# Optimization experiments

Hardware: AMD Instinct MI355X
Metric: run time of the kernel (lower is better)

## Reference

```python
import jax, jax.numpy as jnp
import numpy as np


def setup_inputs() -> dict:
    key = jax.random.key(0)
    ks = jax.random.split(key, 7)
    b, t, c = 2, 2048, 1024
    s = 0.02  # keep pre-softmax logits in a sane range
    return {
        "query": jax.random.normal(ks[0], (b, t, c), jnp.float32),
        "key": jax.random.normal(ks[1], (b, t, c), jnp.float32),
        "value": jax.random.normal(ks[2], (b, t, c), jnp.float32),
        "in_proj_w": jax.random.normal(ks[3], (3 * c, c), jnp.float32) * s,
        "in_proj_b": jax.random.normal(ks[4], (3 * c,), jnp.float32) * s,
        "out_proj_w": jax.random.normal(ks[5], (c, c), jnp.float32) * s,
        "out_proj_b": jax.random.normal(ks[6], (c,), jnp.float32) * s,
        "window_size": 128,
    }


def reference(query, key, value, in_proj_w, in_proj_b, out_proj_w, out_proj_b, window_size):
    num_heads = 16
    b, t, c = query.shape
    hd = c // num_heads
    wq, wk, wv = in_proj_w[:c], in_proj_w[c:2 * c], in_proj_w[2 * c:]
    bq, bk, bv = in_proj_b[:c], in_proj_b[c:2 * c], in_proj_b[2 * c:]
    # project and split heads: [b, h, t, hd]
    q = (query @ wq.T + bq).reshape(b, t, num_heads, hd).transpose(0, 2, 1, 3)
    k = (key @ wk.T + bk).reshape(b, t, num_heads, hd).transpose(0, 2, 1, 3)
    v = (value @ wv.T + bv).reshape(b, t, num_heads, hd).transpose(0, 2, 1, 3)
    # NOTE: torch adds a *float* attn_mask to the logits. The original mask is
    # 1.0 inside the sliding window, 0.0 outside -- an additive +1 bias, NOT -inf.
    idx = jnp.arange(t)
    band = (jnp.abs(idx[:, None] - idx[None, :]) <= window_size).astype(q.dtype)  # [t, t]
    scale = 1.0 / jnp.sqrt(jnp.asarray(hd, q.dtype))
    logits = jnp.einsum("bhqd,bhkd->bhqk", q * scale, k) + band  # [b,h,t,t]
    attn = jax.nn.softmax(logits, axis=-1)
    out = jnp.einsum("bhqk,bhkd->bhqd", attn, v)  # [b,h,t,hd]
    out = out.transpose(0, 2, 1, 3).reshape(b, t, c)
    return out @ out_proj_w.T + out_proj_b
```

## Files before the change

### kernel.cpp

```cpp
#include <hip/hip_runtime.h>

typedef __attribute__((ext_vector_type(8)))  short short8;
typedef __attribute__((ext_vector_type(4)))  float f32x4;
typedef __attribute__((ext_vector_type(16))) float f32x16;
typedef __attribute__((ext_vector_type(2)))  unsigned uint2v;

constexpr int B  = 2;
constexpr int T  = 2048;
constexpr int C  = 1024;
constexpr int H  = 16;
constexpr int HD = 64;

__device__ inline unsigned bf16rne(float a){
  unsigned u = __builtin_bit_cast(unsigned, a);
  u += 0x7fffu + ((u >> 16) & 1u);
  return u >> 16;
}
__device__ inline unsigned bf16pair(float a, float b){
  unsigned ua = __builtin_bit_cast(unsigned, a); ua += 0x7fffu + ((ua >> 16) & 1u);
  unsigned ub = __builtin_bit_cast(unsigned, b); ub += 0x7fffu + ((ub >> 16) & 1u);
  return (ua >> 16) | (ub & 0xffff0000u);
}
__device__ inline void gll16(const void* g, void* l){
  __builtin_amdgcn_global_load_lds(
      (const __attribute__((address_space(1))) unsigned*)g,
      (__attribute__((address_space(3))) unsigned*)l, 16, 0, 0);
}
__device__ inline float exp2f_(float x){
#if __has_builtin(__builtin_amdgcn_exp2f)
  return __builtin_amdgcn_exp2f(x);
#else
  return __builtin_exp2f(x);
#endif
}

__global__ void convert_k(const float* __restrict__ ipw, const float* __restrict__ opw,
                          const float* __restrict__ q, const float* __restrict__ k,
                          const float* __restrict__ v, unsigned* __restrict__ dst)
{
  const int i = blockIdx.x * 256 + threadIdx.x;
  const long e = (long)i * 4;
  const float* src; long off;
  if      (e <  3145728) { src = ipw; off = e; }
  else if (e <  4194304) { src = opw; off = e - 3145728; }
  else if (e <  8388608) { src = q;   off = e - 4194304; }
  else if (e < 12582912) { src = k;   off = e - 8388608; }
  else                   { src = v;   off = e - 12582912; }
  const float4 x = *(const float4*)(src + off);
  dst[i*2+0] = bf16pair(x.x, x.y);
  dst[i*2+1] = bf16pair(x.z, x.w);
}

__global__ __launch_bounds__(256, 3) void gemm_qkv(
    const unsigned short* __restrict__ A0, const unsigned short* __restrict__ A1,
    const unsigned short* __restrict__ A2,
    const unsigned short* __restrict__ Wb, const float* __restrict__ bias,
    unsigned short* __restrict__ Qb, unsigned short* __restrict__ Kf,
    unsigned short* __restrict__ Vf)
{
  __shared__ __align__(16) char gsm[32768];
  unsigned short* As = (unsigned short*)gsm;
  unsigned short* Bs = (unsigned short*)(gsm + 16384);

  const int tid  = threadIdx.x, lane = tid & 63, wv = tid >> 6;
  const int wm   = wv & 1, wn = wv >> 1;
  const int bn   = blockIdx.x, bm = blockIdx.y;
  const int m16  = lane & 15, quad = lane >> 4;

  const int which = bn >> 3;
  const unsigned short* A = (which == 0) ? A0 : (which == 1 ? A1 : A2);

  f32x4 acc[4][4];
#pragma unroll
  for (int i = 0; i < 4; i++)
#pragma unroll
    for (int j = 0; j < 4; j++) acc[i][j] = (f32x4){0.f, 0.f, 0.f, 0.f};

  const int srow = wv * 32 + (lane >> 3);
  const int skp  = (lane & 7) * 8;

  for (int k0 = 0; k0 < 1024; k0 += 64) {
    __syncthreads();
#pragma unroll
    for (int p = 0; p < 4; p++) {
      gll16(A  + (size_t)(bm*128 + srow + p*8)*1024 + k0 + skp, (char*)As + wv*4096 + p*1024);
      gll16(Wb + (size_t)(bn*128 + srow + p*8)*1024 + k0 + skp, (char*)Bs + wv*4096 + p*1024);
    }
    __syncthreads();

#pragma unroll
    for (int kk = 0; kk < 2; kk++) {
      short8 af[4], bf[4];
#pragma unroll
      for (int i = 0; i < 4; i++)
        af[i] = *(const short8*)((const char*)As + (wm*64 + i*16 + m16)*128 + kk*64 + quad*16);
#pragma unroll
      for (int j = 0; j < 4; j++)
        bf[j] = *(const short8*)((const char*)Bs + (wn*64 + j*16 + m16)*128 + kk*64 + quad*16);
#pragma unroll
      for (int i = 0; i < 4; i++)
#pragma unroll
        for (int j = 0; j < 4; j++)
          acc[i][j] = __builtin_amdgcn_mfma_f32_16x16x32_bf16(af[i], bf[j], acc[i][j], 0,0,0);
    }
  }

  __syncthreads();
  float* Ls = (float*)gsm;
  const int hbase = (bn & 7) * 2;
  const int b = bm >> 4;
  const int tbase = (bm & 15) * 128;
  const float ksc = (which == 1) ? 0.18033688f : 1.0f;

  if (which < 2) {
#pragma unroll
    for (int j = 0; j < 4; ++j) {
      const float bj = bias[bn*128 + wn*64 + j*16 + m16] * ksc;
#pragma unroll
      for (int i = 0; i < 4; ++i) {
        const int m0 = wm*64 + i*16 + quad*4;
#pragma unroll
        for (int r = 0; r < 4; ++r)
          Ls[(m0 + r)*36 + wn*16 + m16] = __builtin_fmaf(acc[i][j][r], ksc, bj);
      }
      __syncthreads();
#pragma unroll
      for (int r2 = 0; r2 < 2; ++r2) {
        const int v = r2*256 + tid;
        const int m = v & 127, seg = v >> 7;
        const int wn2 = seg >> 1;
        const float* src = &Ls[m*36 + wn2*16 + (seg & 1)*8];
        const float4 f0 = *(const float4*)src;
        const float4 f1 = *(const float4*)(src + 4);
        uint4 st;
        st.x = bf16pair(f0.x, f0.y); st.y = bf16pair(f0.z, f0.w);
        st.z = bf16pair(f1.x, f1.y); st.w = bf16pair(f1.z, f1.w);
        const int bhh = b*16 + hbase + wn2;
        if (which == 0) {
          const int d0 = j*16 + (seg & 1)*8;
          *(uint4*)&Qb[((size_t)(bhh*2048) + tbase + m)*64 + d0] = st;
        } else {
          const int kt = (tbase + m) >> 6;
          const int wkk = (m >> 5) & 1, ln2 = m & 31;
          const int h2 = seg & 1;
          uint4* dp = (uint4*)Kf + ((size_t)(bhh*32 + kt)*8 + j*2 + wkk)*64 + h2*32 + ln2;
          *dp = st;
        }
      }
      __syncthreads();
    }
  } else {
#pragma unroll
    for (int j = 0; j < 4; ++j) {
      const float bj = bias[bn*128 + wn*64 + j*16 + m16];
      const int col = wn*16 + m16;
#pragma unroll
      for (int i = 0; i < 4; ++i) {
        f32x4 tv = acc[i][j];
        tv[0] += bj; tv[1] += bj; tv[2] += bj; tv[3] += bj;
        *(f32x4*)&Ls[col*132 + wm*64 + i*16 + quad*4] = tv;
      }
      __syncthreads();
#pragma unroll
      for (int r2 = 0; r2 < 2; ++r2) {
        const int v = r2*256 + tid;
        const int n = v >> 4, mseg = v & 15;
        const float* src = &Ls[n*132 + mseg*8];
        const float4 f0 = *(const float4*)src;
        const float4 f1 = *(const float4*)(src + 4);
        uint4 st;
        st.x = bf16pair(f0.x, f0.y); st.y = bf16pair(f0.z, f0.w);
        st.z = bf16pair(f1.x, f1.y); st.w = bf16pair(f1.z, f1.w);
        const int d = j*16 + (n & 15);
        const int bhh = b*16 + hbase + (n >> 4);
        const int t0 = tbase + mseg*8;
        const int kt = t0 >> 6, tc = (t0 & 63) >> 3;
        const int wkk = tc >> 2, cc = (tc >> 1) & 1, h2 = tc & 1;
        const int dt = d >> 5, ln2 = d & 31;
        uint4* dp = (uint4*)Vf + (size_t)(bhh*32 + kt)*512 + dt*256 + cc*128 + wkk*64 + h2*32 + ln2;
        *dp = st;
      }
      __syncthreads();
    }
  }
}

__global__ __launch_bounds__(256, 3) void gemm_out(
    const unsigned short* __restrict__ Ab, const unsigned short* __restrict__ Wb,
    const float* __restrict__ bias, float* __restrict__ outF)
{
  __shared__ __align__(16) char gsm[24576];
  unsigned short* As = (unsigned short*)gsm;
  unsigned short* Ws = (unsigned short*)(gsm + 16384);

  const int tid  = threadIdx.x, lane = tid & 63, wv = tid >> 6;
  const int wm   = wv & 1, wn = wv >> 1;
  const int bn   = blockIdx.x, bm = blockIdx.y;
  const int m16  = lane & 15, quad = lane >> 4;

  f32x4 acc[4][2];
#pragma unroll
  for (int i = 0; i < 4; i++)
#pragma unroll
    for (int j = 0; j < 2; j++) acc[i][j] = (f32x4){0.f, 0.f, 0.f, 0.f};

  const int arow = wv * 32 + (lane >> 3);
  const int wrow = wv * 16 + (lane >> 3);
  const int skp  = (lane & 7) * 8;

  for (int k0 = 0; k0 < 1024; k0 += 64) {
    __syncthreads();
#pragma unroll
    for (int p = 0; p < 4; p++)
      gll16(Ab + (size_t)(bm*128 + arow + p*8)*1024 + k0 + skp, (char*)As + wv*4096 + p*1024);
#pragma unroll
    for (int p = 0; p < 2; p++)
      gll16(Wb + (size_t)(bn*64 + wrow + p*8)*1024 + k0 + skp, (char*)Ws + wv*2048 + p*1024);
    __syncthreads();

#pragma unroll
    for (int kk = 0; kk < 2; kk++) {
      short8 af[4], bf[2];
#pragma unroll
      for (int i = 0; i < 4; i++)
        af[i] = *(const short8*)((const char*)As + (wm*64 + i*16 + m16)*128 + kk*64 + quad*16);
#pragma unroll
      for (int j = 0; j < 2; j++)
        bf[j] = *(const short8*)((const char*)Ws + (wn*32 + j*16 + m16)*128 + kk*64 + quad*16);
#pragma unroll
      for (int i = 0; i < 4; i++)
#pragma unroll
        for (int j = 0; j < 2; j++)
          acc[i][j] = __builtin_amdgcn_mfma_f32_16x16x32_bf16(af[i], bf[j], acc[i][j], 0,0,0);
    }
  }

#pragma unroll
  for (int j = 0; j < 2; j++) {
    const int n_e = bn*64 + wn*32 + j*16 + m16;
    const float bj = bias[n_e];
#pragma unroll
    for (int i = 0; i < 4; i++) {
      const int mbase = bm*128 + wm*64 + i*16 + quad*4;
#pragma unroll
      for (int r = 0; r < 4; r++)
        outF[(size_t)(mbase + r) * 1024 + n_e] = acc[i][j][r] + bj;
    }
  }
}

__global__ __launch_bounds__(256, 3) void attn_k(
    const unsigned short* __restrict__ Qb, const unsigned short* __restrict__ Kf,
    const unsigned short* __restrict__ Vf, const int* __restrict__ wptr,
    unsigned short* __restrict__ ctx)
{
  __shared__ __align__(16) char smem[16896];
  float* Om   = (float*)smem;
  float* lbuf = (float*)(smem + 16384);

  const int tid = threadIdx.x, lane = tid & 63, wv = tid >> 6;
  const int wq = wv >> 1, wk = wv & 1;
  const int h = lane >> 5, ln = lane & 31;
  const int bh = blockIdx.x, qt = blockIdx.y;
  const int win = *wptr;
  const int q0 = qt * 64 + wq * 32;
  const size_t hb = (size_t)bh * T * HD;

  constexpr float LOG2E = 1.44269504f;

  short8 qf[4];
#pragma unroll
  for (int s = 0; s < 4; s++)
    qf[s] = *(const short8*)(Qb + hb + (size_t)(q0 + ln)*64 + s*16 + h*8);

  short8 onesv;
#pragma unroll
  for (int jj = 0; jj < 8; jj++) onesv[jj] = (short)0x3F80;

  f32x16 O0, O1, Lacc, Zv;
#pragma unroll
  for (int r = 0; r < 16; r++) { O0[r] = 0.f; O1[r] = 0.f; Lacc[r] = 0.f; Zv[r] = 0.f; }
  const int tq = q0 + ln;

  const uint4* kbase = (const uint4*)Kf + (size_t)bh*32*512 + wk*64 + lane;
  const uint4* vbase = (const uint4*)Vf + (size_t)bh*32*512 + wk*64 + lane;

  uint4 kA[4], vA[4];
#pragma unroll
  for (int s = 0; s < 4; s++) kA[s] = kbase[s*128];
#pragma unroll
  for (int u = 0; u < 4; u++) vA[u] = vbase[(u >> 1)*256 + (u & 1)*128];

  for (int kt = 0; kt < 32; ++kt) {
    f32x16 st;
#pragma unroll
    for (int s = 0; s < 4; s++) {
      const short8 kf2 = __builtin_bit_cast(short8, kA[s]);
      st = __builtin_amdgcn_mfma_f32_32x32x16_bf16(kf2, qf[s], (s == 0 ? Zv : st), 0, 0, 0);
    }
    if (kt < 31) {
      const size_t o = (size_t)(kt + 1) * 512;
#pragma unroll
      for (int s = 0; s < 4; s++) kA[s] = kbase[o + s*128];
    }

    const int kb = kt*64 + wk*32;
    int sep = 0;
    if (kb > q0 + 31) sep = kb - (q0 + 31);
    else if (q0 > kb + 31) sep = q0 - (kb + 31);
    const int d1 = kb + 31 - q0, d2 = q0 + 31 - kb;
    const int dmax = max(d1 < 0 ? -d1 : d1, d2 < 0 ? -d2 : d2);

    float pr[16];
    if (sep > win) {
#pragma unroll
      for (int r = 0; r < 16; r++) pr[r] = exp2f_(st[r]);
    } else if (dmax <= win) {
#pragma unroll
      for (int r = 0; r < 16; r++) pr[r] = exp2f_(st[r] + LOG2E);
    } else {
      const int tkb = kb + 4*h;
#pragma unroll
      for (int r = 0; r < 16; r++) {
        const int tk = tkb + (r & 3) + 8*(r >> 2);
        int dd = tq - tk; dd = dd < 0 ? -dd : dd;
        pr[r] = exp2f_(st[r] + (dd <= win ? LOG2E : 0.0f));
      }
    }

    unsigned pk[8];
#pragma unroll
    for (int g = 0; g < 8; g++)
      pk[g] = __builtin_amdgcn_perm(__builtin_bit_cast(unsigned, pr[2*g+1]),
                                    __builtin_bit_cast(unsigned, pr[2*g]),
                                    0x07060302u);

#pragma unroll
    for (int c = 0; c < 2; c++) {
      const uint2v s02 = __builtin_amdgcn_permlane32_swap(pk[4*c+0], pk[4*c+2], false, false);
      const uint2v s13 = __builtin_amdgcn_permlane32_swap(pk[4*c+1], pk[4*c+3], false, false);
      union { unsigned u[4]; short8 v; } P;
      P.u[0] = s02[0];
      P.u[1] = s13[0];
      P.u[2] = s02[1];
      P.u[3] = s13[1];
#pragma unroll
      for (int dt = 0; dt < 2; dt++) {
        const short8 vf2 = __builtin_bit_cast(short8, vA[dt*2 + c]);
        if (dt == 0) O0 = __builtin_amdgcn_mfma_f32_32x32x16_bf16(P.v, vf2, O0, 0,0,0);
        else         O1 = __builtin_amdgcn_mfma_f32_32x32x16_bf16(P.v, vf2, O1, 0,0,0);
      }
      Lacc = __builtin_amdgcn_mfma_f32_32x32x16_bf16(P.v, onesv, Lacc, 0,0,0);
    }

    if (kt < 31) {
      const size_t o = (size_t)(kt + 1) * 512;
#pragma unroll
      for (int u = 0; u < 4; u++) vA[u] = vbase[o + (u >> 1)*256 + (u & 1)*128];
    }
  }

  __syncthreads();
  if (wk == 1) {
#pragma unroll
    for (int r = 0; r < 16; r++) {
      Om[wq*2048 + r*64 + lane]        = O0[r];
      Om[wq*2048 + (16 + r)*64 + lane] = O1[r];
    }
    if (ln == 0) {
#pragma unroll
      for (int r = 0; r < 16; r++)
        lbuf[wq*32 + (r & 3) + 8*(r >> 2) + 4*h] = Lacc[r];
    }
  }
  __syncthreads();
  if (wk == 0) {
    const int b = bh >> 4, hh = bh & 15;
#pragma unroll
    for (int r = 0; r < 16; r++) {
      const int qrow = (r & 3) + 8*(r >> 2) + 4*h;
      const float lt = Lacc[r] + lbuf[wq*32 + qrow];
      const float linv = 1.0f / lt;
      const int t = q0 + qrow;
      const float o0 = (O0[r] + Om[wq*2048 + r*64 + lane]) * linv;
      const float o1 = (O1[r] + Om[wq*2048 + (16 + r)*64 + lane]) * linv;
      unsigned short* cp = ctx + (size_t)(b*2048 + t)*1024 + hh*64;
      cp[ln]      = (unsigned short)bf16rne(o0);
      cp[32 + ln] = (unsigned short)bf16rne(o1);
    }
  }
}

extern "C" void kernel_launch(void* const* d_in, const int* in_sizes, int n_in,
                              void* d_out, int out_size, void* d_ws, size_t ws_size,
                              hipStream_t stream)
{
  const float* query = (const float*)d_in[0];
  const float* key   = (const float*)d_in[1];
  const float* value = (const float*)d_in[2];
  const float* ipw   = (const float*)d_in[3];
  const float* ipb   = (const float*)d_in[4];
  const float* opw   = (const float*)d_in[5];
  const float* opb   = (const float*)d_in[6];
  const int*   win   = (const int*)d_in[7];

  char* ws = (char*)d_ws;
  unsigned short* Winbf  = (unsigned short*)(ws);
  unsigned short* Woutbf = (unsigned short*)(ws + 6291456);
  unsigned short* Qin    = (unsigned short*)(ws + 8388608);
  unsigned short* Kin    = (unsigned short*)(ws + 16777216);
  unsigned short* Vin    = (unsigned short*)(ws + 25165824);
  unsigned short* Qb     = (unsigned short*)(ws + 33554432);
  unsigned short* Kf     = (unsigned short*)(ws + 41943040);
  unsigned short* Vf     = (unsigned short*)(ws + 50331648);
  unsigned short* ctx    = (unsigned short*)(ws + 58720256);

  convert_k<<<16384, 256, 0, stream>>>(ipw, opw, query, key, value, (unsigned*)ws);

  gemm_qkv<<<dim3(24, 32), 256, 0, stream>>>(
      Qin, Kin, Vin, Winbf, ipb, Qb, Kf, Vf);

  attn_k<<<dim3(32, 32), 256, 0, stream>>>(Qb, Kf, Vf, win, ctx);

  gemm_out<<<dim3(16, 32), 256, 0, stream>>>(
      ctx, Woutbf, opb, (float*)d_out);
}
```

Before: 221.0 us.

## Widen convert stores, shrink out-proj GEMM tiles, split attention launch by batch

The conversion kernel now processes 8 floats per thread and writes one 16-byte store, halving the grid. The output projection GEMM moves from 128x64 to 64x64 tiles with each wave owning a 16-column strip, which doubles the block count and cuts LDS so 4 blocks fit per CU. The attention launch is split into two launches of 16 batch-heads each via an offset argument. Smaller GEMM tiles improve occupancy and wave balance but lower per-block data reuse, and the extra attention launch adds launch overhead.

```diff
diff --git a/kernel.cpp b/kernel.cpp
--- a/kernel.cpp
+++ b/kernel.cpp
@@ -39,16 +39,19 @@
                           const float* __restrict__ v, unsigned* __restrict__ dst)
 {
   const int i = blockIdx.x * 256 + threadIdx.x;
-  const long e = (long)i * 4;
+  const long e = (long)i * 8;
   const float* src; long off;
   if      (e <  3145728) { src = ipw; off = e; }
   else if (e <  4194304) { src = opw; off = e - 3145728; }
   else if (e <  8388608) { src = q;   off = e - 4194304; }
   else if (e < 12582912) { src = k;   off = e - 8388608; }
   else                   { src = v;   off = e - 12582912; }
-  const float4 x = *(const float4*)(src + off);
-  dst[i*2+0] = bf16pair(x.x, x.y);
-  dst[i*2+1] = bf16pair(x.z, x.w);
+  const float4 x0 = *(const float4*)(src + off);
+  const float4 x1 = *(const float4*)(src + off + 4);
+  uint4 st;
+  st.x = bf16pair(x0.x, x0.y); st.y = bf16pair(x0.z, x0.w);
+  st.z = bf16pair(x1.x, x1.y); st.w = bf16pair(x1.z, x1.w);
+  *(uint4*)(dst + (size_t)i*4) = st;
 }
 
 __global__ __launch_bounds__(256, 3) void gemm_qkv(
@@ -185,74 +188,62 @@
   }
 }
 
-__global__ __launch_bounds__(256, 3) void gemm_out(
+__global__ __launch_bounds__(256, 4) void gemm_out(
     const unsigned short* __restrict__ Ab, const unsigned short* __restrict__ Wb,
     const float* __restrict__ bias, float* __restrict__ outF)
 {
-  __shared__ __align__(16) char gsm[24576];
+  __shared__ __align__(16) char gsm[16384];
   unsigned short* As = (unsigned short*)gsm;
-  unsigned short* Ws = (unsigned short*)(gsm + 16384);
+  unsigned short* Ws = (unsigned short*)(gsm + 8192);
 
   const int tid  = threadIdx.x, lane = tid & 63, wv = tid >> 6;
-  const int wm   = wv & 1, wn = wv >> 1;
   const int bn   = blockIdx.x, bm = blockIdx.y;
   const int m16  = lane & 15, quad = lane >> 4;
 
-  f32x4 acc[4][2];
-#pragma unroll
-  for (int i = 0; i < 4; i++)
-#pragma unroll
-    for (int j = 0; j < 2; j++) acc[i][j] = (f32x4){0.f, 0.f, 0.f, 0.f};
-
-  const int arow = wv * 32 + (lane >> 3);
-  const int wrow = wv * 16 + (lane >> 3);
+  f32x4 acc[4];
+#pragma unroll
+  for (int i = 0; i < 4; i++) acc[i] = (f32x4){0.f, 0.f, 0.f, 0.f};
+
+  const int srow = wv * 16 + (lane >> 3);
   const int skp  = (lane & 7) * 8;
 
   for (int k0 = 0; k0 < 1024; k0 += 64) {
     __syncthreads();
 #pragma unroll
-    for (int p = 0; p < 4; p++)
-      gll16(Ab + (size_t)(bm*128 + arow + p*8)*1024 + k0 + skp, (char*)As + wv*4096 + p*1024);
-#pragma unroll
-    for (int p = 0; p < 2; p++)
-      gll16(Wb + (size_t)(bn*64 + wrow + p*8)*1024 + k0 + skp, (char*)Ws + wv*2048 + p*1024);
+    for (int p = 0; p < 2; p++) {
+      gll16(Ab + (size_t)(bm*64 + srow + p*8)*1024 + k0 + skp, (char*)As + wv*2048 + p*1024);
+      gll16(Wb + (size_t)(bn*64 + srow + p*8)*1024 + k0 + skp, (char*)Ws + wv*2048 + p*1024);
+    }
     __syncthreads();
 
 #pragma unroll
     for (int kk = 0; kk < 2; kk++) {
-      short8 af[4], bf[2];
+      short8 af[4], bf;
 #pragma unroll
       for (int i = 0; i < 4; i++)
-        af[i] = *(const short8*)((const char*)As + (wm*64 + i*16 + m16)*128 + kk*64 + quad*16);
-#pragma unroll
-      for (int j = 0; j < 2; j++)
-        bf[j] = *(const short8*)((const char*)Ws + (wn*32 + j*16 + m16)*128 + kk*64 + quad*16);
+        af[i] = *(const short8*)((const char*)As + (i*16 + m16)*128 + kk*64 + quad*16);
+      bf = *(const short8*)((const char*)Ws + (wv*16 + m16)*128 + kk*64 + quad*16);
 #pragma unroll
       for (int i = 0; i < 4; i++)
-#pragma unroll
-        for (int j = 0; j < 2; j++)
-          acc[i][j] = __builtin_amdgcn_mfma_f32_16x16x32_bf16(af[i], bf[j], acc[i][j], 0,0,0);
-    }
-  }
-
-#pragma unroll
-  for (int j = 0; j < 2; j++) {
-    const int n_e = bn*64 + wn*32 + j*16 + m16;
-    const float bj = bias[n_e];
-#pragma unroll
-    for (int i = 0; i < 4; i++) {
-      const int mbase = bm*128 + wm*64 + i*16 + quad*4;
-#pragma unroll
-      for (int r = 0; r < 4; r++)
-        outF[(size_t)(mbase + r) * 1024 + n_e] = acc[i][j][r] + bj;
-    }
+        acc[i] = __builtin_amdgcn_mfma_f32_16x16x32_bf16(af[i], bf, acc[i], 0,0,0);
+    }
+  }
+
+  const int n_e = bn*64 + wv*16 + m16;
+  const float bj = bias[n_e];
+#pragma unroll
+  for (int i = 0; i < 4; i++) {
+    const int mbase = bm*64 + i*16 + quad*4;
+#pragma unroll
+    for (int r = 0; r < 4; r++)
+      outF[(size_t)(mbase + r) * 1024 + n_e] = acc[i][r] + bj;
   }
 }
 
 __global__ __launch_bounds__(256, 3) void attn_k(
     const unsigned short* __restrict__ Qb, const unsigned short* __restrict__ Kf,
     const unsigned short* __restrict__ Vf, const int* __restrict__ wptr,
-    unsigned short* __restrict__ ctx)
+    unsigned short* __restrict__ ctx, int bh0)
 {
   __shared__ __align__(16) char smem[16896];
   float* Om   = (float*)smem;
@@ -261,7 +252,7 @@
   const int tid = threadIdx.x, lane = tid & 63, wv = tid >> 6;
   const int wq = wv >> 1, wk = wv & 1;
   const int h = lane >> 5, ln = lane & 31;
-  const int bh = blockIdx.x, qt = blockIdx.y;
+  const int bh = bh0 + blockIdx.x, qt = blockIdx.y;
   const int win = *wptr;
   const int q0 = qt * 64 + wq * 32;
   const size_t hb = (size_t)bh * T * HD;
@@ -415,13 +406,14 @@
   unsigned short* Vf     = (unsigned short*)(ws + 50331648);
   unsigned short* ctx    = (unsigned short*)(ws + 58720256);
 
-  convert_k<<<16384, 256, 0, stream>>>(ipw, opw, query, key, value, (unsigned*)ws);
+  convert_k<<<8192, 256, 0, stream>>>(ipw, opw, query, key, value, (unsigned*)ws);
 
   gemm_qkv<<<dim3(24, 32), 256, 0, stream>>>(
       Qin, Kin, Vin, Winbf, ipb, Qb, Kf, Vf);
 
-  attn_k<<<dim3(32, 32), 256, 0, stream>>>(Qb, Kf, Vf, win, ctx);
-
-  gemm_out<<<dim3(16, 32), 256, 0, stream>>>(
+  attn_k<<<dim3(16, 32), 256, 0, stream>>>(Qb, Kf, Vf, win, ctx, 0);
+  attn_k<<<dim3(16, 32), 256, 0, stream>>>(Qb, Kf, Vf, win, ctx, 16);
+
+  gemm_out<<<dim3(16, 64), 256, 0, stream>>>(
       ctx, Woutbf, opb, (float*)d_out);
 }
```

New measurement: 223.5 us. No clear change (+1.1%).
